# Optimization experiments

Measured on AMD Instinct MI355X. Metric: run time of the kernel, lower is better.

## Reference

```python
import jax, jax.numpy as jnp
import numpy as np

INPUT_DIM = 1024
OUTPUT_DIM = 1000
DEPTH = 10
LAMBDA_REG = 1e-3
N_INTERNAL = 2 ** DEPTH - 1
N_LEAF = 2 ** DEPTH
BATCH = 16384


def setup_inputs() -> dict:
    key = jax.random.key(0)
    k1, k2, k3 = jax.random.split(key, 3)
    X = jax.random.normal(k1, (BATCH, INPUT_DIM), dtype=jnp.float32)
    # torch nn.Linear weight layout: [out_features, in_features]; scaled to keep
    # sigmoid routing probs away from 0/1 saturation (log-reg term).
    W_internal = jax.random.normal(k2, (N_INTERNAL, INPUT_DIM + 1), dtype=jnp.float32) * 0.02
    W_leaf = jax.random.normal(k3, (OUTPUT_DIM, N_LEAF), dtype=jnp.float32) * 0.02
    return {"X": X, "W_internal": W_internal, "W_leaf": W_leaf}


def _tree_paths(X, W_internal):
    B = X.shape[0]
    Xb = jnp.concatenate([jnp.ones((B, 1), X.dtype), X], axis=1)  # [B, D+1]
    logits = jax.nn.sigmoid(Xb @ W_internal.T)                    # [B, N_int]
    routing = jnp.stack([logits, 1.0 - logits], axis=2)           # [B, N_int, 2]
    path = jnp.ones((B, 1), X.dtype)
    reg = jnp.float32(0.0)
    start = 0
    for layer in range(DEPTH):
        n = 2 ** layer
        lp = routing[:, start:start + n, :].reshape(B, 2 * n)     # next_paths [B, 2n]
        path = jnp.repeat(path, 2, axis=1) * lp                   # new path probs [B, 2n]
        # Faithful to source: parent_idx = node_idx // 2 indexes the UPDATED path probs.
        parent = jnp.repeat(path[:, :n], 2, axis=1)               # [B, 2n]
        num = jnp.sum(lp * parent, axis=0)                        # [2n]
        den = jnp.sum(parent, axis=0) + 1e-8                      # [2n]
        alpha = num / den
        factor = LAMBDA_REG * 2.0 ** (-layer)
        reg = reg + factor * jnp.sum(-0.5 * (jnp.log(alpha) + jnp.log(1.0 - alpha)))
        start += n
    return path, reg  # path: [B, 2^DEPTH]


def reference(X, W_internal, W_leaf):
    path_probs, reg = _tree_paths(X, W_internal)
    predictions = path_probs @ W_leaf.T   # [B, output_dim]
    return predictions, reg
```

## Files before the change

kernel.cpp:

```cpp
#include <hip/hip_runtime.h>
#include <hip/hip_bf16.h>

#define B_ROWS 16384
#define K_DIM  1024
#define N_INT  1023
#define N_OUT  1000

using s8vec = __attribute__((ext_vector_type(8))) short;
using f32x4 = __attribute__((ext_vector_type(4))) float;

static const size_t OFF_XB   = 0;
static const size_t OFF_W1   = OFF_XB   + 33554432;
static const size_t OFF_BIAS = OFF_W1   + 2097152;
static const size_t OFF_PROB = OFF_BIAS + 4096;
static const size_t OFF_PATH = OFF_PROB + 33554432;
static const size_t OFF_W2   = OFF_PATH + 33554432;
static const size_t OFF_SG   = OFF_W2   + 2097152;

__device__ __forceinline__ float b2f(ushort u) {
  return __uint_as_float(((unsigned)u) << 16);
}
__device__ __forceinline__ float blo(unsigned u) { return __uint_as_float(u << 16); }
__device__ __forceinline__ float bhi(unsigned u) { return __uint_as_float(u & 0xffff0000u); }
__device__ __forceinline__ ushort f2b(float f) {
  unsigned u = __float_as_uint(f);
  u = u + 0x7FFFu + ((u >> 16) & 1u);
  return (ushort)(u >> 16);
}

__global__ __launch_bounds__(256) void cvt_x(const float4* __restrict__ X,
                                             ushort4* __restrict__ O) {
  const int i = blockIdx.x * 256 + threadIdx.x;
  const float4 v = X[i];
  ushort4 o;
  o.x = f2b(v.x); o.y = f2b(v.y); o.z = f2b(v.z); o.w = f2b(v.w);
  O[i] = o;
}

__global__ __launch_bounds__(256) void cvt_w(const float* __restrict__ Wi,
                                             const float* __restrict__ Wl,
                                             ushort* __restrict__ W1,
                                             ushort* __restrict__ W2,
                                             float* __restrict__ bias) {
  const int idx = blockIdx.x * 256 + threadIdx.x;
  if (idx < (1 << 20)) {
    const int n = idx >> 10, k = idx & 1023;
    const float v = (n < N_INT) ? Wi[n * 1025 + 1 + k] : 0.f;
    W1[idx] = f2b(v);
    if (k == 0) bias[n] = (n < N_INT) ? Wi[n * 1025] : 0.f;
  } else {
    const int j = idx - (1 << 20);
    const int n = j >> 10, k = j & 1023;
    const float v = (n < N_OUT) ? Wl[n * 1024 + k] : 0.f;
    W2[j] = f2b(v);
  }
}

template <int MODE>
__global__ __launch_bounds__(256, 4) void gemm_bt(const ushort* __restrict__ A,
                                                  const ushort* __restrict__ Bm,
                                                  const float* __restrict__ bias,
                                                  void* __restrict__ outp) {
  __shared__ ushort As[2][4096];
  __shared__ ushort Bs[2][4096];
  const int tid = threadIdx.x;
  const int bn = blockIdx.x, bm = blockIdx.y;
  const int lane = tid & 63, wv = tid >> 6;
  const int wm = wv >> 1, wn = wv & 1;
  const int m16 = lane & 15, q = lane >> 4;

  const ushort* a0p = A  + (size_t)(bm * 128 + (tid >> 2)) * 1024 + (tid & 3) * 8;
  const ushort* b0p = Bm + (size_t)(bn * 128 + (tid >> 2)) * 1024 + (tid & 3) * 8;

  f32x4 acc[4][4] = {};

  {
    uint4 ra0 = *(const uint4*)(a0p);
    uint4 ra1 = *(const uint4*)(a0p + 65536);
    uint4 rb0 = *(const uint4*)(b0p);
    uint4 rb1 = *(const uint4*)(b0p + 65536);
    *(uint4*)(As[0] + tid * 8)        = ra0;
    *(uint4*)(As[0] + 2048 + tid * 8) = ra1;
    *(uint4*)(Bs[0] + tid * 8)        = rb0;
    *(uint4*)(Bs[0] + 2048 + tid * 8) = rb1;
  }

  for (int k0 = 0; k0 < 1024; k0 += 32) {
    const int cur = (k0 >> 5) & 1;
    const int nxt = cur ^ 1;
    uint4 ra0, ra1, rb0, rb1;
    const bool more = (k0 + 32) < 1024;
    if (more) {
      ra0 = *(const uint4*)(a0p + k0 + 32);
      ra1 = *(const uint4*)(a0p + 65536 + k0 + 32);
      rb0 = *(const uint4*)(b0p + k0 + 32);
      rb1 = *(const uint4*)(b0p + 65536 + k0 + 32);
    }
    __syncthreads();
    if (more) {
      *(uint4*)(As[nxt] + tid * 8)        = ra0;
      *(uint4*)(As[nxt] + 2048 + tid * 8) = ra1;
      *(uint4*)(Bs[nxt] + tid * 8)        = rb0;
      *(uint4*)(Bs[nxt] + 2048 + tid * 8) = rb1;
    }
    s8vec af[4], bfv[4];
#pragma unroll
    for (int i = 0; i < 4; ++i)
      af[i] = *(const s8vec*)(As[cur] + (wm * 64 + i * 16 + m16) * 32 + q * 8);
#pragma unroll
    for (int j = 0; j < 4; ++j)
      bfv[j] = *(const s8vec*)(Bs[cur] + (wn * 64 + j * 16 + m16) * 32 + q * 8);
#pragma unroll
    for (int i = 0; i < 4; ++i)
#pragma unroll
      for (int j = 0; j < 4; ++j)
        acc[i][j] = __builtin_amdgcn_mfma_f32_16x16x32_bf16(af[i], bfv[j], acc[i][j], 0, 0, 0);
  }

  if (MODE == 0) {
    ushort* P = (ushort*)outp;
#pragma unroll
    for (int i = 0; i < 4; ++i)
#pragma unroll
      for (int r = 0; r < 4; ++r) {
        const int gr = bm * 128 + wm * 64 + i * 16 + q * 4 + r;
#pragma unroll
        for (int j = 0; j < 4; ++j) {
          const int gc = bn * 128 + wn * 64 + j * 16 + m16;
          const float z = acc[i][j][r] + bias[gc];
          const float p = 1.f / (1.f + expf(-z));
          if (gc < N_INT) P[(size_t)gr * 1024 + gc + 1] = f2b(p);
        }
      }
  } else {
    float* O = (float*)outp;
#pragma unroll
    for (int i = 0; i < 4; ++i)
#pragma unroll
      for (int r = 0; r < 4; ++r) {
        const int gr = bm * 128 + wm * 64 + i * 16 + q * 4 + r;
#pragma unroll
        for (int j = 0; j < 4; ++j) {
          const int gc = bn * 128 + wn * 64 + j * 16 + m16;
          if (gc < N_OUT) O[(size_t)gr * 1000 + gc] = acc[i][j][r];
        }
      }
  }
}

__global__ __launch_bounds__(256) void tree_kernel(const ushort* __restrict__ probs,
                                                   ushort* __restrict__ path,
                                                   float* __restrict__ Sg) {
  __shared__ float Ss[4096];
  for (int i = threadIdx.x; i < 4096; i += 256) Ss[i] = 0.f;
  __syncthreads();
  const int lane = threadIdx.x & 63;
  const int gw = blockIdx.x * 4 + (threadIdx.x >> 6);

  float at1[6] = {}, at2[6] = {};
  float ae1[30] = {}, ae2[30] = {};

#pragma unroll 1
  for (int rr = 0; rr < 4; ++rr) {
    const int r = gw * 4 + rr;
    const ushort* prow = probs + (size_t)r * 1024;
    const ushort p6 = prow[64 + lane];
    const uint   p7 = *(const uint*)(prow + 128 + 2 * lane);
    const uint2  p8 = *(const uint2*)(prow + 256 + 4 * lane);
    const uint4  p9 = *(const uint4*)(prow + 512 + 8 * lane);

    float v = 1.f;
#pragma unroll
    for (int t = 1; t <= 6; ++t) {
      const int ell = t - 1;
      const int e = lane >> (6 - t);
      const float p = b2f(prow[(1 << ell) + (e >> 1)]);
      v *= (e & 1) ? (1.f - p) : p;
      if (((lane & ((1 << (6 - t)) - 1)) == 0) && (e < (1 << ell))) {
        const float pj = b2f(prow[(1 << ell) + e]);
        at1[ell] += v;
        at2[ell] += pj * v;
      }
    }

    float w[16];
    {
      const float p = b2f(p6);
      w[1] = v * (1.f - p); w[0] = v * p;
    }
    {
      const int j0 = __shfl((int)p6, 2 * lane);
      const int j1 = __shfl((int)p6, 2 * lane + 1);
      if (lane < 32) {
        ae1[0] += w[0]; ae2[0] += b2f((ushort)j0) * w[0];
        ae1[1] += w[1]; ae2[1] += b2f((ushort)j1) * w[1];
      }
    }
    {
      const float pA = blo(p7), pB = bhi(p7);
      w[3] = w[1] * (1.f - pB); w[2] = w[1] * pB;
      w[1] = w[0] * (1.f - pA); w[0] = w[0] * pA;
    }
    {
      const uint ua = (uint)__shfl((int)p7, 2 * lane);
      const uint ub = (uint)__shfl((int)p7, 2 * lane + 1);
      if (lane < 32) {
        ae1[2] += w[0]; ae2[2] += blo(ua) * w[0];
        ae1[3] += w[1]; ae2[3] += bhi(ua) * w[1];
        ae1[4] += w[2]; ae2[4] += blo(ub) * w[2];
        ae1[5] += w[3]; ae2[5] += bhi(ub) * w[3];
      }
    }
    {
      const float pv[4] = { blo(p8.x), bhi(p8.x), blo(p8.y), bhi(p8.y) };
#pragma unroll
      for (int i = 3; i >= 0; --i) {
        w[2 * i + 1] = w[i] * (1.f - pv[i]);
        w[2 * i]     = w[i] * pv[i];
      }
    }
    {
      const uint u0 = (uint)__shfl((int)p8.x, 2 * lane);
      const uint u1 = (uint)__shfl((int)p8.y, 2 * lane);
      const uint u2 = (uint)__shfl((int)p8.x, 2 * lane + 1);
      const uint u3 = (uint)__shfl((int)p8.y, 2 * lane + 1);
      if (lane < 32) {
        ae1[6]  += w[0]; ae2[6]  += blo(u0) * w[0];
        ae1[7]  += w[1]; ae2[7]  += bhi(u0) * w[1];
        ae1[8]  += w[2]; ae2[8]  += blo(u1) * w[2];
        ae1[9]  += w[3]; ae2[9]  += bhi(u1) * w[3];
        ae1[10] += w[4]; ae2[10] += blo(u2) * w[4];
        ae1[11] += w[5]; ae2[11] += bhi(u2) * w[5];
        ae1[12] += w[6]; ae2[12] += blo(u3) * w[6];
        ae1[13] += w[7]; ae2[13] += bhi(u3) * w[7];
      }
    }
    {
      const uint pv[4] = { p9.x, p9.y, p9.z, p9.w };
#pragma unroll
      for (int i = 7; i >= 0; --i) {
        const float p = (i & 1) ? bhi(pv[i >> 1]) : blo(pv[i >> 1]);
        w[2 * i + 1] = w[i] * (1.f - p);
        w[2 * i]     = w[i] * p;
      }
    }
    {
      uint s_[8];
      s_[0] = (uint)__shfl((int)p9.x, 2 * lane);
      s_[1] = (uint)__shfl((int)p9.y, 2 * lane);
      s_[2] = (uint)__shfl((int)p9.z, 2 * lane);
      s_[3] = (uint)__shfl((int)p9.w, 2 * lane);
      s_[4] = (uint)__shfl((int)p9.x, 2 * lane + 1);
      s_[5] = (uint)__shfl((int)p9.y, 2 * lane + 1);
      s_[6] = (uint)__shfl((int)p9.z, 2 * lane + 1);
      s_[7] = (uint)__shfl((int)p9.w, 2 * lane + 1);
      if (lane < 32) {
#pragma unroll
        for (int i = 0; i < 16; ++i) {
          const uint u = s_[i >> 1];
          const float pj = (i & 1) ? bhi(u) : blo(u);
          ae1[14 + i] += w[i]; ae2[14 + i] += pj * w[i];
        }
      }
    }
    union { ushort u[16]; uint4 q4[2]; } pk;
#pragma unroll
    for (int i = 0; i < 16; ++i) pk.u[i] = f2b(w[i]);
    uint4* dst = (uint4*)(path + (size_t)r * 1024 + lane * 16);
    dst[0] = pk.q4[0];
    dst[1] = pk.q4[1];
  }

#pragma unroll
  for (int t = 1; t <= 6; ++t) {
    const int ell = t - 1;
    const int e = lane >> (6 - t);
    if (((lane & ((1 << (6 - t)) - 1)) == 0) && (e < (1 << ell))) {
      const int node = (1 << ell) - 1 + e;
      atomicAdd(&Ss[node], at1[ell]);
      atomicAdd(&Ss[2048 + node], at2[ell]);
    }
  }
  if (lane < 32) {
#pragma unroll
    for (int ell = 6; ell <= 9; ++ell) {
      const int s = 1 << (ell - 6);
      const int pb = (1 << ell) - 1;
      const int base = 2 * s - 2;
#pragma unroll
      for (int i = 0; i < 2 * s; ++i) {
        const int node = pb + 2 * s * lane + i;
        atomicAdd(&Ss[node], ae1[base + i]);
        atomicAdd(&Ss[2048 + node], ae2[base + i]);
      }
    }
  }
  __syncthreads();
  for (int i = threadIdx.x; i < 1023; i += 256) {
    atomicAdd(&Sg[i], Ss[i]);
    atomicAdd(&Sg[2048 + i], Ss[2048 + i]);
  }
}

__global__ __launch_bounds__(1024) void finalize_kernel(const float* __restrict__ Sg,
                                                        float* __restrict__ outreg) {
  const int tid = threadIdx.x;
  double val = 0.0;
  if (tid < 1023) {
    const int ell = 31 - __clz(tid + 1);
    const double s1 = (double)Sg[tid];
    const double s2 = (double)Sg[2048 + tid];
    const double den = s1 + 1e-8;
    const double a0 = s2 / den;
    const double a1 = (s1 - s2) / den;
    const double f = 1e-3 * (1.0 / (double)(1 << ell));
    val = -0.5 * f * (log(a0) + log(1.0 - a0) + log(a1) + log(1.0 - a1));
  }
#pragma unroll
  for (int o = 32; o > 0; o >>= 1) val += __shfl_down(val, o, 64);
  __shared__ double partd[16];
  if ((tid & 63) == 0) partd[tid >> 6] = val;
  __syncthreads();
  if (tid == 0) {
    double t = 0.0;
    for (int i = 0; i < 16; ++i) t += partd[i];
    outreg[0] = (float)t;
  }
}

extern "C" void kernel_launch(void* const* d_in, const int* in_sizes, int n_in,
                              void* d_out, int out_size, void* d_ws, size_t ws_size,
                              hipStream_t stream) {
  const float* X     = (const float*)d_in[0];
  const float* Wint  = (const float*)d_in[1];
  const float* Wleaf = (const float*)d_in[2];
  float* out = (float*)d_out;
  char* ws = (char*)d_ws;

  ushort* Xb   = (ushort*)(ws + OFF_XB);
  ushort* W1   = (ushort*)(ws + OFF_W1);
  float*  bias = (float*)(ws + OFF_BIAS);
  ushort* prob = (ushort*)(ws + OFF_PROB);
  ushort* path = (ushort*)(ws + OFF_PATH);
  ushort* W2   = (ushort*)(ws + OFF_W2);
  float*  Sg   = (float*)(ws + OFF_SG);

  (void)hipMemsetAsync(ws + OFF_SG, 0, 16384, stream);
  cvt_x<<<16384, 256, 0, stream>>>((const float4*)X, (ushort4*)Xb);
  cvt_w<<<8192, 256, 0, stream>>>(Wint, Wleaf, W1, W2, bias);
  gemm_bt<0><<<dim3(8, 128), 256, 0, stream>>>(Xb, W1, bias, (void*)prob);
  tree_kernel<<<1024, 256, 0, stream>>>(prob, path, Sg);
  gemm_bt<1><<<dim3(8, 128), 256, 0, stream>>>(path, W2, nullptr, (void*)out);
  finalize_kernel<<<1, 1024, 0, stream>>>(Sg, out + (size_t)B_ROWS * N_OUT);
}
```

Measured before the change: 326.3 us.

## Merge conversion kernels, fold finalize into tree kernel, prefetch next prob row

Folds the memset and both conversion kernels into one launch, which now also zeroes the accumulator and a completion counter. The finalize kernel is absorbed into tree_kernel: the last block to finish, detected with an atomic counter and threadfences, computes the regularizer. tree_kernel also prefetches the next row's probabilities into registers and replaces scalar global loads for the top levels with lane shuffles. This cuts launch count and load latency, at the cost of relying on last-block-done ordering and a little extra register pressure.

```diff
diff --git a/kernel.cpp b/kernel.cpp
--- a/kernel.cpp
+++ b/kernel.cpp
@@ -28,31 +28,36 @@
   return (ushort)(u >> 16);
 }
 
-__global__ __launch_bounds__(256) void cvt_x(const float4* __restrict__ X,
-                                             ushort4* __restrict__ O) {
-  const int i = blockIdx.x * 256 + threadIdx.x;
-  const float4 v = X[i];
-  ushort4 o;
-  o.x = f2b(v.x); o.y = f2b(v.y); o.z = f2b(v.z); o.w = f2b(v.w);
-  O[i] = o;
-}
-
-__global__ __launch_bounds__(256) void cvt_w(const float* __restrict__ Wi,
-                                             const float* __restrict__ Wl,
-                                             ushort* __restrict__ W1,
-                                             ushort* __restrict__ W2,
-                                             float* __restrict__ bias) {
-  const int idx = blockIdx.x * 256 + threadIdx.x;
-  if (idx < (1 << 20)) {
-    const int n = idx >> 10, k = idx & 1023;
-    const float v = (n < N_INT) ? Wi[n * 1025 + 1 + k] : 0.f;
-    W1[idx] = f2b(v);
-    if (k == 0) bias[n] = (n < N_INT) ? Wi[n * 1025] : 0.f;
+__global__ __launch_bounds__(256) void cvt_all(const float4* __restrict__ X,
+                                               const float* __restrict__ Wi,
+                                               const float* __restrict__ Wl,
+                                               ushort4* __restrict__ Xb,
+                                               ushort* __restrict__ W1,
+                                               ushort* __restrict__ W2,
+                                               float* __restrict__ bias,
+                                               float* __restrict__ Sg) {
+  const int bid = blockIdx.x;
+  if (bid < 16384) {
+    const int i = bid * 256 + threadIdx.x;
+    const float4 v = X[i];
+    ushort4 o;
+    o.x = f2b(v.x); o.y = f2b(v.y); o.z = f2b(v.z); o.w = f2b(v.w);
+    Xb[i] = o;
+  } else if (bid < 24576) {
+    const int idx = (bid - 16384) * 256 + threadIdx.x;
+    if (idx < (1 << 20)) {
+      const int n = idx >> 10, k = idx & 1023;
+      const float v = (n < N_INT) ? Wi[n * 1025 + 1 + k] : 0.f;
+      W1[idx] = f2b(v);
+      if (k == 0) bias[n] = (n < N_INT) ? Wi[n * 1025] : 0.f;
+    } else {
+      const int j = idx - (1 << 20);
+      const int n = j >> 10, k = j & 1023;
+      const float v = (n < N_OUT) ? Wl[n * 1024 + k] : 0.f;
+      W2[j] = f2b(v);
+    }
   } else {
-    const int j = idx - (1 << 20);
-    const int n = j >> 10, k = j & 1023;
-    const float v = (n < N_OUT) ? Wl[n * 1024 + k] : 0.f;
-    W2[j] = f2b(v);
+    for (int i = threadIdx.x; i < 4097; i += 256) Sg[i] = 0.f;
   }
 }
 
@@ -150,7 +155,8 @@
 
 __global__ __launch_bounds__(256) void tree_kernel(const ushort* __restrict__ probs,
                                                    ushort* __restrict__ path,
-                                                   float* __restrict__ Sg) {
+                                                   float* __restrict__ Sg,
+                                                   float* __restrict__ outreg) {
   __shared__ float Ss[4096];
   for (int i = threadIdx.x; i < 4096; i += 256) Ss[i] = 0.f;
   __syncthreads();
@@ -160,24 +166,36 @@
   float at1[6] = {}, at2[6] = {};
   float ae1[30] = {}, ae2[30] = {};
 
+  const ushort* prow0 = probs + (size_t)(gw * 4) * 1024;
+  int  c_l64 = prow0[lane];
+  int  c_p6  = prow0[64 + lane];
+  uint c_p7  = *(const uint*)(prow0 + 128 + 2 * lane);
+  uint2 c_p8 = *(const uint2*)(prow0 + 256 + 4 * lane);
+  uint4 c_p9 = *(const uint4*)(prow0 + 512 + 8 * lane);
+
 #pragma unroll 1
   for (int rr = 0; rr < 4; ++rr) {
     const int r = gw * 4 + rr;
-    const ushort* prow = probs + (size_t)r * 1024;
-    const ushort p6 = prow[64 + lane];
-    const uint   p7 = *(const uint*)(prow + 128 + 2 * lane);
-    const uint2  p8 = *(const uint2*)(prow + 256 + 4 * lane);
-    const uint4  p9 = *(const uint4*)(prow + 512 + 8 * lane);
+    const int l64 = c_l64, p6i = c_p6;
+    const uint p7 = c_p7; const uint2 p8 = c_p8; const uint4 p9 = c_p9;
+    if (rr < 3) {
+      const ushort* pn = probs + (size_t)(r + 1) * 1024;
+      c_l64 = pn[lane];
+      c_p6  = pn[64 + lane];
+      c_p7  = *(const uint*)(pn + 128 + 2 * lane);
+      c_p8  = *(const uint2*)(pn + 256 + 4 * lane);
+      c_p9  = *(const uint4*)(pn + 512 + 8 * lane);
+    }
 
     float v = 1.f;
 #pragma unroll
     for (int t = 1; t <= 6; ++t) {
       const int ell = t - 1;
       const int e = lane >> (6 - t);
-      const float p = b2f(prow[(1 << ell) + (e >> 1)]);
+      const float p = b2f((ushort)__shfl(l64, (1 << ell) + (e >> 1)));
       v *= (e & 1) ? (1.f - p) : p;
+      const float pj = b2f((ushort)__shfl(l64, (1 << ell) + e));
       if (((lane & ((1 << (6 - t)) - 1)) == 0) && (e < (1 << ell))) {
-        const float pj = b2f(prow[(1 << ell) + e]);
         at1[ell] += v;
         at2[ell] += pj * v;
       }
@@ -185,12 +203,12 @@
 
     float w[16];
     {
-      const float p = b2f(p6);
+      const float p = b2f((ushort)p6i);
       w[1] = v * (1.f - p); w[0] = v * p;
     }
     {
-      const int j0 = __shfl((int)p6, 2 * lane);
-      const int j1 = __shfl((int)p6, 2 * lane + 1);
+      const int j0 = __shfl(p6i, 2 * lane);
+      const int j1 = __shfl(p6i, 2 * lane + 1);
       if (lane < 32) {
         ae1[0] += w[0]; ae2[0] += b2f((ushort)j0) * w[0];
         ae1[1] += w[1]; ae2[1] += b2f((ushort)j1) * w[1];
@@ -300,31 +318,37 @@
     atomicAdd(&Sg[i], Ss[i]);
     atomicAdd(&Sg[2048 + i], Ss[2048 + i]);
   }
-}
-
-__global__ __launch_bounds__(1024) void finalize_kernel(const float* __restrict__ Sg,
-                                                        float* __restrict__ outreg) {
-  const int tid = threadIdx.x;
-  double val = 0.0;
-  if (tid < 1023) {
-    const int ell = 31 - __clz(tid + 1);
-    const double s1 = (double)Sg[tid];
-    const double s2 = (double)Sg[2048 + tid];
-    const double den = s1 + 1e-8;
-    const double a0 = s2 / den;
-    const double a1 = (s1 - s2) / den;
-    const double f = 1e-3 * (1.0 / (double)(1 << ell));
-    val = -0.5 * f * (log(a0) + log(1.0 - a0) + log(a1) + log(1.0 - a1));
-  }
-#pragma unroll
-  for (int o = 32; o > 0; o >>= 1) val += __shfl_down(val, o, 64);
-  __shared__ double partd[16];
-  if ((tid & 63) == 0) partd[tid >> 6] = val;
+
+  __threadfence();
+  __shared__ unsigned last;
+  if (threadIdx.x == 0)
+    last = atomicAdd((unsigned*)(Sg + 4096), 1u);
   __syncthreads();
-  if (tid == 0) {
-    double t = 0.0;
-    for (int i = 0; i < 16; ++i) t += partd[i];
-    outreg[0] = (float)t;
+  if (last == gridDim.x - 1) {
+    __threadfence();
+    const int tid = threadIdx.x;
+    double val = 0.0;
+#pragma unroll
+    for (int s = 0; s < 4; ++s) {
+      const int node = tid + s * 256;
+      if (node < 1023) {
+        const int ell = 31 - __clz(node + 1);
+        const double s1 = (double)Sg[node];
+        const double s2 = (double)Sg[2048 + node];
+        const double den = s1 + 1e-8;
+        const double a0 = s2 / den;
+        const double a1 = (s1 - s2) / den;
+        const double f = 1e-3 * (1.0 / (double)(1 << ell));
+        val += -0.5 * f * (log(a0) + log(1.0 - a0) + log(a1) + log(1.0 - a1));
+      }
+    }
+#pragma unroll
+    for (int o = 32; o > 0; o >>= 1) val += __shfl_down(val, o, 64);
+    __shared__ double partd[4];
+    if ((tid & 63) == 0) partd[tid >> 6] = val;
+    __syncthreads();
+    if (tid == 0)
+      outreg[0] = (float)(partd[0] + partd[1] + partd[2] + partd[3]);
   }
 }
 
@@ -345,11 +369,9 @@
   ushort* W2   = (ushort*)(ws + OFF_W2);
   float*  Sg   = (float*)(ws + OFF_SG);
 
-  (void)hipMemsetAsync(ws + OFF_SG, 0, 16384, stream);
-  cvt_x<<<16384, 256, 0, stream>>>((const float4*)X, (ushort4*)Xb);
-  cvt_w<<<8192, 256, 0, stream>>>(Wint, Wleaf, W1, W2, bias);
+  cvt_all<<<24577, 256, 0, stream>>>((const float4*)X, Wint, Wleaf,
+                                     (ushort4*)Xb, W1, W2, bias, Sg);
   gemm_bt<0><<<dim3(8, 128), 256, 0, stream>>>(Xb, W1, bias, (void*)prob);
-  tree_kernel<<<1024, 256, 0, stream>>>(prob, path, Sg);
+  tree_kernel<<<1024, 256, 0, stream>>>(prob, path, Sg, out + (size_t)B_ROWS * N_OUT);
   gemm_bt<1><<<dim3(8, 128), 256, 0, stream>>>(path, W2, nullptr, (void*)out);
-  finalize_kernel<<<1, 1024, 0, stream>>>(Sg, out + (size_t)B_ROWS * N_OUT);
-}
+}
```

New measurement: 394.4 us. +20.8%, slower.
